# Kernel tuning notes

Measured on AMD Instinct MI355X. Metric: run time of the kernel, lower is better.

The kernel has to match this reference:

```python
import jax, jax.numpy as jnp
import numpy as np

OUT = 7  # STN crop size hard-coded as (7, 7) in the original build()


def gather_pairs(num_points):
    # replicates the pred_gather_indexes construction in build()
    pairs = [[0, 0]]
    si = 1
    while si + 2 < num_points:
        pairs.append([si, si])
        pairs.append([si + 1, si + 2])
        si += 3
    pairs.append([si, si])
    pairs.append([si + 1, si + 1])
    return np.asarray(pairs, dtype=np.int32)


def _sample_one(feat, theta):
    # feat [H,W,C], theta [6] = affine row-major 2x3; classic STN bilinear crop
    H, W, _ = feat.shape
    lin = jnp.linspace(-1.0, 1.0, OUT)
    gy, gx = jnp.meshgrid(lin, lin, indexing='ij')
    xs = theta[0] * gx + theta[1] * gy + theta[2]
    ys = theta[3] * gx + theta[4] * gy + theta[5]
    px = (xs + 1.0) * (W - 1) * 0.5
    py = (ys + 1.0) * (H - 1) * 0.5
    x0 = jnp.floor(px)
    y0 = jnp.floor(py)
    wx = px - x0
    wy = py - y0
    x0i = jnp.clip(x0, 0, W - 1).astype(jnp.int32)
    x1i = jnp.clip(x0 + 1, 0, W - 1).astype(jnp.int32)
    y0i = jnp.clip(y0, 0, H - 1).astype(jnp.int32)
    y1i = jnp.clip(y0 + 1, 0, H - 1).astype(jnp.int32)
    Ia = feat[y0i, x0i]
    Ib = feat[y1i, x0i]
    Ic = feat[y0i, x1i]
    Id = feat[y1i, x1i]
    wa = ((1 - wx) * (1 - wy))[..., None]
    wb = ((1 - wx) * wy)[..., None]
    wc = (wx * (1 - wy))[..., None]
    wd = (wx * wy)[..., None]
    return wa * Ia + wb * Ib + wc * Ic + wd * Id  # [OUT,OUT,C]

# vmap over boxes then over batch -> feat [B,H,W,C], theta [B,n,6] -> [B,n,7,7,C]
_sample = jax.vmap(jax.vmap(_sample_one, in_axes=(None, 0)), in_axes=(0, 0))


def _hierarchy(pred_prev, feat, W1, b1, W2, b2, W3, b3):
    B = pred_prev.shape[0]
    centers = (pred_prev[:, :-1] + pred_prev[:, 1:]) * 0.5
    diffs = (pred_prev[:, 1:] - pred_prev[:, :-1]) * 0.5
    cx, cy = centers[..., 0], centers[..., 1]
    dx, dy = diffs[..., 0], diffs[..., 1]
    # fixed (non-trainable) dense with constant kernel -> theta = [dx,-dy,-cx,dy,dx,-cy]
    theta = jnp.stack([dx, -dy, -cx, dy, dx, -cy], axis=-1)  # [B,n,6]
    theta = jax.lax.stop_gradient(theta)  # stop_gradient=True default
    rois = _sample(feat, theta)  # [B,n,7,7,C]
    n = theta.shape[1]
    x = rois.reshape(B * n, -1)
    f1 = jnp.tanh(x @ W1 + b1)
    f2 = jnp.tanh(f1 @ W2 + b2)
    f3 = f2 @ W3 + b3 + jnp.asarray([-1.0, 0.0, 0.0, 0.0, 1.0, 0.0], dtype=f2.dtype)
    npnt = n * 3
    pts = f3.reshape(B, npnt, 2)
    # fixed homography dense: (x,y) -> (x,y,-1)
    hom = jnp.concatenate([pts, -jnp.ones((B, npnt, 1), dtype=pts.dtype)], axis=-1)
    theta_e = jnp.repeat(theta, 3, axis=1).reshape(B, npnt, 2, 3)
    pt = jnp.einsum('bpij,bpj->bpi', theta_e, hom)  # [B,npnt,2]
    idx = gather_pairs(npnt)  # [m,2]
    pg = pt[:, idx]  # [B,m,2,2]
    return pg.mean(axis=2)  # [B,m,2]


def setup_inputs() -> dict:
    key = jax.random.key(0)
    ks = jax.random.split(key, 16)
    B = 32
    d = {
        'last_feature': jax.random.normal(ks[0], (B, 4096), jnp.float32),
        'conv4_3': jax.random.normal(ks[1], (B, 28, 28, 512), jnp.float32),
        'conv3_3': jax.random.normal(ks[2], (B, 56, 56, 256), jnp.float32),
        'conv2_2': jax.random.normal(ks[3], (B, 112, 112, 128), jnp.float32),
        'W_trans': jax.random.normal(ks[4], (4096, 18), jnp.float32) * 0.005,
        'b_trans': jnp.zeros((18,), jnp.float32),
    }
    C = [512, 256, 128]
    for h in range(3):
        kk = jax.random.split(ks[5 + h], 3)
        fan = OUT * OUT * C[h]
        d[f'W1_{h}'] = jax.random.normal(kk[0], (fan, 1024), jnp.float32) * 0.001
        d[f'b1_{h}'] = jnp.zeros((1024,), jnp.float32)
        d[f'W2_{h}'] = jax.random.normal(kk[1], (1024, 256), jnp.float32) * 0.02
        d[f'b2_{h}'] = jnp.zeros((256,), jnp.float32)
        d[f'W3_{h}'] = jax.random.normal(kk[2], (256, 6), jnp.float32) * 0.01
        d[f'b3_{h}'] = jnp.zeros((6,), jnp.float32)
    return d


def reference(last_feature, conv4_3, conv3_3, conv2_2, W_trans, b_trans,
              W1_0, b1_0, W2_0, b2_0, W3_0, b3_0,
              W1_1, b1_1, W2_1, b2_1, W3_1, b3_1,
              W1_2, b1_2, W2_2, b2_2, W3_2, b3_2):
    B = last_feature.shape[0]
    pred = (last_feature @ W_trans + b_trans).reshape(B, 9, 2)
    feats = [conv4_3, conv3_3, conv2_2]
    heads = [(W1_0, b1_0, W2_0, b2_0, W3_0, b3_0),
             (W1_1, b1_1, W2_1, b2_1, W3_1, b3_1),
             (W1_2, b1_2, W2_2, b2_2, W3_2, b3_2)]
    for h in range(3):
        pred = _hierarchy(pred, feats[h], *heads[h])
    return pred[:, :-1, :] * 6.0  # [B,64,2]
```

## Files before the change

kernel.cpp:

```cpp
#include <hip/hip_runtime.h>
#include <hip/hip_bf16.h>
#include <math.h>

typedef __attribute__((ext_vector_type(8))) short   short8;
typedef __attribute__((ext_vector_type(4))) float   floatx4;

#define OFF_PRED     0ULL
#define OFF_PTA      16384ULL
#define OFF_PTB      65536ULL
#define OFF_W2T      131072ULL
#define OFF_F1       2097152ULL
#define OFF_P2       4194304ULL
#define OFF_X        16777216ULL
#define OFF_P1       33554432ULL
#define OFF_W1T      67108864ULL

__device__ inline void pair_idx(int p, int Pn, int npnt, int& i1, int& i2) {
    if (p == 0) { i1 = i2 = 0; }
    else if (p >= Pn - 2) { i1 = i2 = npnt - (Pn - p); }
    else {
        int q = (p - 1) >> 1, r = (p - 1) & 1;
        int si = 1 + 3 * q;
        if (r == 0) { i1 = i2 = si; } else { i1 = si + 1; i2 = si + 2; }
    }
}
__device__ inline float2 pred_point(const float* pred0, const float* pt,
                                    int nsegP, int b, int p) {
    if (nsegP == 0) {
        const float* q = pred0 + ((size_t)b * 9 + p) * 2;
        return float2{q[0], q[1]};
    }
    int npnt = nsegP * 3, Pn = 2 * nsegP + 1;
    int i1, i2; pair_idx(p, Pn, npnt, i1, i2);
    const float* a = pt + ((size_t)b * npnt + i1) * 2;
    const float* c = pt + ((size_t)b * npnt + i2) * 2;
    return float2{0.5f * (a[0] + c[0]), 0.5f * (a[1] + c[1])};
}

struct SetupArgs {
    const float* W1s[3]; __hip_bfloat16* W1T[3]; int K[3];
    const float* W2s[3]; __hip_bfloat16* W2T[3];
    const float* lf; const float* Wt; const float* bt; float* pred;
};

__device__ inline void transpose_tile(const float* __restrict__ src,
                                      __hip_bfloat16* __restrict__ dst,
                                      int R, int C, int rowT, int colT,
                                      float (*tile)[33]) {
    int tx = threadIdx.x & 31, ty = threadIdx.x >> 5;
    int r0 = rowT * 32, c0 = colT * 32;
    #pragma unroll
    for (int k = 0; k < 4; ++k)
        tile[ty + k * 8][tx] = src[(size_t)(r0 + ty + k * 8) * C + c0 + tx];
    __syncthreads();
    #pragma unroll
    for (int k = 0; k < 4; ++k)
        dst[(size_t)(c0 + ty + k * 8) * R + r0 + tx] =
            __float2bfloat16(tile[tx][ty + k * 8]);
}

__global__ __launch_bounds__(256) void setup_kernel(SetupArgs a) {
    __shared__ float tile[32][33];
    int id = blockIdx.x;
    if (id < 43904) {
        int h = (id < 25088) ? 0 : (id < 37632 ? 1 : 2);
        int base = (h == 0) ? 0 : (h == 1 ? 25088 : 37632);
        int l = id - base;
        transpose_tile(a.W1s[h], a.W1T[h], a.K[h], 1024, l >> 5, l & 31, tile);
    } else if (id < 44672) {
        int l = id - 43904;
        int h = l >> 8; int t = l & 255;
        transpose_tile(a.W2s[h], a.W2T[h], 1024, 256, t >> 3, t & 7, tile);
    } else {
        int l = id - 44672;
        int wave = threadIdx.x >> 6, lane = threadIdx.x & 63;
        int task = l * 4 + wave;
        int j = task % 18, b = task / 18;
        const float* lfb = a.lf + (size_t)b * 4096;
        float acc = 0.f;
        for (int k = lane; k < 4096; k += 64)
            acc += lfb[k] * a.Wt[(size_t)k * 18 + j];
        #pragma unroll
        for (int off = 32; off >= 1; off >>= 1)
            acc += __shfl_xor(acc, off, 64);
        if (lane == 0) a.pred[b * 18 + j] = acc + a.bt[j];
    }
}

__global__ __launch_bounds__(256) void sample_kernel(
    const float* __restrict__ feat, int Wd, int lc,
    const float* __restrict__ pred0, const float* __restrict__ ptPrev, int nsegP,
    int lns, __hip_bfloat16* __restrict__ x)
{
    int nseg = 1 << lns;
    int blk = blockIdx.x;
    int i = blk & (nseg - 1), b = blk >> lns;
    float2 p0 = pred_point(pred0, ptPrev, nsegP, b, i);
    float2 p1 = pred_point(pred0, ptPrev, nsegP, b, i + 1);
    float cx = 0.5f * (p0.x + p1.x), cy = 0.5f * (p0.y + p1.y);
    float dx = 0.5f * (p1.x - p0.x), dy = 0.5f * (p1.y - p0.y);

    __shared__ float4 wv[49];
    __shared__ int4   ov[49];
    int t = threadIdx.x;
    int C = 1 << lc;
    if (t < 49) {
        int oy = t / 7, ox = t - oy * 7;
        float gx = (float)(ox - 3) * (1.f / 3.f);
        float gy = (float)(oy - 3) * (1.f / 3.f);
        float xs = dx * gx - dy * gy - cx;
        float ys = dy * gx + dx * gy - cy;
        float fW = (float)(Wd - 1);
        float px = (xs + 1.f) * fW * 0.5f;
        float py = (ys + 1.f) * fW * 0.5f;
        float x0f = floorf(px), y0f = floorf(py);
        float wx = px - x0f, wy = py - y0f;
        int xi0 = (int)fminf(fmaxf(x0f,       0.f), fW);
        int xi1 = (int)fminf(fmaxf(x0f + 1.f, 0.f), fW);
        int yi0 = (int)fminf(fmaxf(y0f,       0.f), fW);
        int yi1 = (int)fminf(fmaxf(y0f + 1.f, 0.f), fW);
        int c4 = C >> 2;
        ov[t] = int4{(yi0 * Wd + xi0) * c4, (yi1 * Wd + xi0) * c4,
                     (yi0 * Wd + xi1) * c4, (yi1 * Wd + xi1) * c4};
        wv[t] = float4{(1.f - wx) * (1.f - wy), (1.f - wx) * wy,
                       wx * (1.f - wy),         wx * wy};
    }
    __syncthreads();

    const float4* fb4 = (const float4*)(feat + (size_t)b * Wd * Wd * C);
    int c4 = 1 << (lc - 2);
    int total4 = 49 << (lc - 2);
    size_t rowbase = (size_t)blk * (49 << lc);
    for (int j = t; j < total4; j += 256) {
        int pix = j >> (lc - 2);
        int cc  = j & (c4 - 1);
        int4 o = ov[pix]; float4 w = wv[pix];
        float4 Ia = fb4[o.x + cc], Ib = fb4[o.y + cc];
        float4 Ic = fb4[o.z + cc], Id = fb4[o.w + cc];
        float4 v;
        v.x = w.x * Ia.x + w.y * Ib.x + w.z * Ic.x + w.w * Id.x;
        v.y = w.x * Ia.y + w.y * Ib.y + w.z * Ic.y + w.w * Id.y;
        v.z = w.x * Ia.z + w.y * Ib.z + w.z * Ic.z + w.w * Id.z;
        v.w = w.x * Ia.w + w.y * Ib.w + w.z * Ic.w + w.w * Id.w;
        __hip_bfloat16 h0 = __float2bfloat16(v.x), h1 = __float2bfloat16(v.y);
        __hip_bfloat16 h2 = __float2bfloat16(v.z), h3 = __float2bfloat16(v.w);
        ushort4 u = {*(unsigned short*)&h0, *(unsigned short*)&h1,
                     *(unsigned short*)&h2, *(unsigned short*)&h3};
        *(ushort4*)(x + rowbase + ((size_t)pix << lc) + cc * 4) = u;
    }
}

__global__ __launch_bounds__(256) void gemm_mfma4(
    const __hip_bfloat16* __restrict__ A, const __hip_bfloat16* __restrict__ Bt,
    float* __restrict__ P, int M, int N, int K, int slice)
{
    int lane = threadIdx.x & 63;
    int wave = threadIdx.x >> 6;
    int lo = lane & 15, hi = lane >> 4;
    int mt = blockIdx.x, nt = blockIdx.y * 4 + wave, s = blockIdx.z;
    const short* Ap = (const short*)A + (size_t)(mt * 64 + lo) * K + (size_t)s * slice + hi * 8;
    const short* Bp = (const short*)Bt + (size_t)(nt * 64 + lo) * K + (size_t)s * slice + hi * 8;

    floatx4 acc[4][4];
    #pragma unroll
    for (int a = 0; a < 4; ++a)
        #pragma unroll
        for (int b = 0; b < 4; ++b)
            acc[a][b] = floatx4{0.f, 0.f, 0.f, 0.f};

    short8 ca[4], cb[4], na[4], nb[4];
    int nch = slice >> 5;

#define LDF(da, db, koff)                                                     \
    {                                                                         \
        _Pragma("unroll")                                                     \
        for (int q = 0; q < 4; ++q)                                           \
            da[q] = *(const short8*)(Ap + (size_t)q * 16 * K + (koff));       \
        _Pragma("unroll")                                                     \
        for (int q = 0; q < 4; ++q)                                           \
            db[q] = *(const short8*)(Bp + (size_t)q * 16 * K + (koff));       \
    }
#define MM(da, db)                                                            \
    {                                                                         \
        _Pragma("unroll")                                                     \
        for (int mi = 0; mi < 4; ++mi)                                        \
            _Pragma("unroll")                                                 \
            for (int ni = 0; ni < 4; ++ni)                                    \
                acc[mi][ni] = __builtin_amdgcn_mfma_f32_16x16x32_bf16(        \
                    da[mi], db[ni], acc[mi][ni], 0, 0, 0);                    \
    }

    LDF(ca, cb, 0)
    for (int c = 0; c + 1 < nch; c += 2) {
        LDF(na, nb, (c + 1) * 32)
        MM(ca, cb)
        if (c + 2 < nch) LDF(ca, cb, (c + 2) * 32)
        MM(na, nb)
    }
    if (nch & 1) MM(ca, cb)

    #pragma unroll
    for (int mi = 0; mi < 4; ++mi) {
        int row0 = mt * 64 + mi * 16 + hi * 4;
        #pragma unroll
        for (int ni = 0; ni < 4; ++ni) {
            int col = nt * 64 + ni * 16 + lo;
            #pragma unroll
            for (int r = 0; r < 4; ++r)
                P[((size_t)s * M + row0 + r) * N + col] = acc[mi][ni][r];
        }
    }
#undef LDF
#undef MM
}

__global__ __launch_bounds__(256) void reduce_tanh_kernel(
    const float* __restrict__ P1, const float* __restrict__ b1,
    __hip_bfloat16* __restrict__ f1, int M, int S)
{
    int e = blockIdx.x * 256 + threadIdx.x;
    int n = e & 1023;
    float v = b1[n];
    size_t stride = (size_t)M * 1024;
    for (int s = 0; s < S; ++s) v += P1[(size_t)s * stride + e];
    f1[e] = __float2bfloat16(tanhf(v));
}

__global__ __launch_bounds__(64) void gemm3pts_kernel(
    const float* __restrict__ P2, const float* __restrict__ b2,
    const float* __restrict__ W3, const float* __restrict__ b3,
    const float* __restrict__ pred0, const float* __restrict__ ptPrev, int nsegP,
    float* __restrict__ pt, int lns, int M)
{
    int m = blockIdx.x;
    int lane = threadIdx.x;
    int nseg = 1 << lns;
    float acc[6] = {0.f, 0.f, 0.f, 0.f, 0.f, 0.f};
    #pragma unroll
    for (int q = 0; q < 4; ++q) {
        int k = lane + q * 64;
        float v = b2[k];
        #pragma unroll
        for (int s = 0; s < 8; ++s)
            v += P2[((size_t)s * M + m) * 256 + k];
        v = tanhf(v);
        const float* w = W3 + (size_t)k * 6;
        #pragma unroll
        for (int j = 0; j < 6; ++j) acc[j] += v * w[j];
    }
    #pragma unroll
    for (int j = 0; j < 6; ++j)
        #pragma unroll
        for (int off = 32; off >= 1; off >>= 1)
            acc[j] += __shfl_xor(acc[j], off, 64);
    if (lane == 0) {
        int i = m & (nseg - 1);
        int b = m >> lns;
        float2 p0 = pred_point(pred0, ptPrev, nsegP, b, i);
        float2 p1 = pred_point(pred0, ptPrev, nsegP, b, i + 1);
        float cx = 0.5f * (p0.x + p1.x), cy = 0.5f * (p0.y + p1.y);
        float dx = 0.5f * (p1.x - p0.x), dy = 0.5f * (p1.y - p0.y);
        float f[6];
        #pragma unroll
        for (int j = 0; j < 6; ++j) f[j] = acc[j] + b3[j];
        f[0] -= 1.f;
        f[4] += 1.f;
        int npnt = nseg * 3;
        size_t base = ((size_t)b * npnt + 3 * i) * 2;
        #pragma unroll
        for (int s = 0; s < 3; ++s) {
            float px = f[2 * s], py = f[2 * s + 1];
            pt[base + 2 * s]     = dx * px - dy * py + cx;
            pt[base + 2 * s + 1] = dy * px + dx * py + cy;
        }
    }
}

__global__ __launch_bounds__(256) void pairs_final_kernel(
    const float* __restrict__ pt, float* __restrict__ outp, int nsegP)
{
    int npnt = nsegP * 3;
    int Pn = 2 * nsegP + 1;
    int idx = blockIdx.x * 256 + threadIdx.x;
    int total = 32 * Pn * 2;
    if (idx >= total) return;
    int c = idx & 1;
    int t = idx >> 1;
    int p = t % Pn, b = t / Pn;
    int i1, i2; pair_idx(p, Pn, npnt, i1, i2);
    float v = 0.5f * (pt[((size_t)b * npnt + i1) * 2 + c] +
                      pt[((size_t)b * npnt + i2) * 2 + c]);
    if (p < Pn - 1) outp[((size_t)b * (Pn - 1) + p) * 2 + c] = 6.f * v;
}

extern "C" void kernel_launch(void* const* d_in, const int* in_sizes, int n_in,
                              void* d_out, int out_size, void* d_ws, size_t ws_size,
                              hipStream_t stream) {
    (void)in_sizes; (void)n_in; (void)out_size; (void)ws_size;
    const float* feats[3] = {(const float*)d_in[1], (const float*)d_in[2], (const float*)d_in[3]};

    char* ws = (char*)d_ws;
    float* predA = (float*)(ws + OFF_PRED);
    float* ptA   = (float*)(ws + OFF_PTA);
    float* ptB   = (float*)(ws + OFF_PTB);
    __hip_bfloat16* f1 = (__hip_bfloat16*)(ws + OFF_F1);
    float* P2          = (float*)(ws + OFF_P2);
    __hip_bfloat16* xb = (__hip_bfloat16*)(ws + OFF_X);
    float* P1          = (float*)(ws + OFF_P1);

    const int Ks[3]  = {25088, 12544, 6272};
    const int S1s[3] = {28, 14, 7};
    const int lcs[3] = {9, 8, 7};
    const int Hs[3]  = {28, 56, 112};
    const int lnss[3] = {3, 4, 5};

    SetupArgs sa;
    size_t w1off = 0;
    for (int h = 0; h < 3; ++h) {
        sa.W1s[h] = (const float*)d_in[6 + 6 * h];
        sa.W1T[h] = (__hip_bfloat16*)(ws + OFF_W1T + w1off);
        sa.K[h]   = Ks[h];
        w1off += (size_t)Ks[h] * 1024 * 2;
        sa.W2s[h] = (const float*)d_in[8 + 6 * h];
        sa.W2T[h] = (__hip_bfloat16*)(ws + OFF_W2T + (size_t)h * 524288);
    }
    sa.lf = (const float*)d_in[0];
    sa.Wt = (const float*)d_in[4];
    sa.bt = (const float*)d_in[5];
    sa.pred = predA;

    setup_kernel<<<dim3(44816), 256, 0, stream>>>(sa);

    float* pts[2] = {ptA, ptB};
    const float* ptPrev = nullptr;
    int nsegP = 0;
    for (int h = 0; h < 3; ++h) {
        int lns = lnss[h], nseg = 1 << lns, M = 32 * nseg;
        int K = Ks[h], S1 = S1s[h];
        const float* b1 = (const float*)d_in[7 + 6 * h];
        const float* b2 = (const float*)d_in[9 + 6 * h];
        const float* W3 = (const float*)d_in[10 + 6 * h];
        const float* b3 = (const float*)d_in[11 + 6 * h];

        sample_kernel<<<dim3(32 * nseg), 256, 0, stream>>>(
            feats[h], Hs[h], lcs[h], predA, ptPrev, nsegP, lns, xb);

        gemm_mfma4<<<dim3(M / 64, 4, S1), 256, 0, stream>>>(
            xb, sa.W1T[h], P1, M, 1024, K, K / S1);

        reduce_tanh_kernel<<<dim3(M * 1024 / 256), 256, 0, stream>>>(P1, b1, f1, M, S1);

        gemm_mfma4<<<dim3(M / 64, 1, 8), 256, 0, stream>>>(
            f1, sa.W2T[h], P2, M, 256, 1024, 128);

        float* ptCur = pts[h & 1];
        gemm3pts_kernel<<<dim3(M), 64, 0, stream>>>(
            P2, b2, W3, b3, predA, ptPrev, nsegP, ptCur, lns, M);

        ptPrev = ptCur; nsegP = nseg;
    }

    pairs_final_kernel<<<dim3((32 * 65 * 2 + 255) / 256), 256, 0, stream>>>(
        ptA, (float*)d_out, 32);
}
```

Before: 777.6 us.

## Triple-buffer GEMM loads, split sampling grid, vectorize reduce, pack gemm3 waves

The main GEMM moves from double to triple register buffering and raises wave priority around each MFMA burst, aiming to hide more global-load latency. The sample kernel splits each box's pixel-channel loop across a second grid dimension to get more blocks in flight. The split-K reduction now reads and writes four elements per thread with float4/ushort4 accesses, and gemm3pts packs four rows per 256-thread block. The extra buffers raise register pressure, which may lower occupancy, and the sample split recomputes the per-pixel offsets and weights in every block.

```diff
diff --git a/kernel.cpp b/kernel.cpp
--- a/kernel.cpp
+++ b/kernel.cpp
@@ -130,8 +130,10 @@
     const float4* fb4 = (const float4*)(feat + (size_t)b * Wd * Wd * C);
     int c4 = 1 << (lc - 2);
     int total4 = 49 << (lc - 2);
+    int chunk = total4 / gridDim.y;
+    int j0 = blockIdx.y * chunk;
     size_t rowbase = (size_t)blk * (49 << lc);
-    for (int j = t; j < total4; j += 256) {
+    for (int j = j0 + t; j < j0 + chunk; j += 256) {
         int pix = j >> (lc - 2);
         int cc  = j & (c4 - 1);
         int4 o = ov[pix]; float4 w = wv[pix];
@@ -168,7 +170,7 @@
         for (int b = 0; b < 4; ++b)
             acc[a][b] = floatx4{0.f, 0.f, 0.f, 0.f};
 
-    short8 ca[4], cb[4], na[4], nb[4];
+    short8 a0[4], b0[4], a1[4], b1[4], a2[4], b2[4];
     int nch = slice >> 5;
 
 #define LDF(da, db, koff)                                                     \
@@ -182,22 +184,46 @@
     }
 #define MM(da, db)                                                            \
     {                                                                         \
+        __builtin_amdgcn_s_setprio(1);                                        \
         _Pragma("unroll")                                                     \
         for (int mi = 0; mi < 4; ++mi)                                        \
             _Pragma("unroll")                                                 \
             for (int ni = 0; ni < 4; ++ni)                                    \
                 acc[mi][ni] = __builtin_amdgcn_mfma_f32_16x16x32_bf16(        \
                     da[mi], db[ni], acc[mi][ni], 0, 0, 0);                    \
-    }
-
-    LDF(ca, cb, 0)
-    for (int c = 0; c + 1 < nch; c += 2) {
-        LDF(na, nb, (c + 1) * 32)
-        MM(ca, cb)
-        if (c + 2 < nch) LDF(ca, cb, (c + 2) * 32)
-        MM(na, nb)
-    }
-    if (nch & 1) MM(ca, cb)
+        __builtin_amdgcn_s_setprio(0);                                        \
+    }
+
+    LDF(a0, b0, 0)
+    if (nch >= 2) LDF(a1, b1, 32)
+    int c = 0;
+    for (; c + 5 < nch; c += 3) {
+        LDF(a2, b2, (c + 2) * 32)
+        MM(a0, b0)
+        LDF(a0, b0, (c + 3) * 32)
+        MM(a1, b1)
+        LDF(a1, b1, (c + 4) * 32)
+        MM(a2, b2)
+    }
+    int r = nch - c;
+    if (r == 1) { MM(a0, b0) }
+    else if (r == 2) { MM(a0, b0) MM(a1, b1) }
+    else if (r == 3) {
+        LDF(a2, b2, (c + 2) * 32)
+        MM(a0, b0) MM(a1, b1) MM(a2, b2)
+    } else if (r == 4) {
+        LDF(a2, b2, (c + 2) * 32)
+        MM(a0, b0)
+        LDF(a0, b0, (c + 3) * 32)
+        MM(a1, b1) MM(a2, b2) MM(a0, b0)
+    } else {
+        LDF(a2, b2, (c + 2) * 32)
+        MM(a0, b0)
+        LDF(a0, b0, (c + 3) * 32)
+        MM(a1, b1)
+        LDF(a1, b1, (c + 4) * 32)
+        MM(a2, b2) MM(a0, b0) MM(a1, b1)
+    }
 
     #pragma unroll
     for (int mi = 0; mi < 4; ++mi) {
@@ -206,8 +232,8 @@
         for (int ni = 0; ni < 4; ++ni) {
             int col = nt * 64 + ni * 16 + lo;
             #pragma unroll
-            for (int r = 0; r < 4; ++r)
-                P[((size_t)s * M + row0 + r) * N + col] = acc[mi][ni][r];
+            for (int r2 = 0; r2 < 4; ++r2)
+                P[((size_t)s * M + row0 + r2) * N + col] = acc[mi][ni][r2];
         }
     }
 #undef LDF
@@ -218,22 +244,32 @@
     const float* __restrict__ P1, const float* __restrict__ b1,
     __hip_bfloat16* __restrict__ f1, int M, int S)
 {
-    int e = blockIdx.x * 256 + threadIdx.x;
-    int n = e & 1023;
-    float v = b1[n];
+    size_t e = ((size_t)blockIdx.x * 256 + threadIdx.x) * 4;
+    int n = (int)(e & 1023);
+    float4 v = *(const float4*)(b1 + n);
     size_t stride = (size_t)M * 1024;
-    for (int s = 0; s < S; ++s) v += P1[(size_t)s * stride + e];
-    f1[e] = __float2bfloat16(tanhf(v));
-}
-
-__global__ __launch_bounds__(64) void gemm3pts_kernel(
+    for (int s = 0; s < S; ++s) {
+        float4 p = *(const float4*)(P1 + (size_t)s * stride + e);
+        v.x += p.x; v.y += p.y; v.z += p.z; v.w += p.w;
+    }
+    __hip_bfloat16 h0 = __float2bfloat16(tanhf(v.x));
+    __hip_bfloat16 h1 = __float2bfloat16(tanhf(v.y));
+    __hip_bfloat16 h2 = __float2bfloat16(tanhf(v.z));
+    __hip_bfloat16 h3 = __float2bfloat16(tanhf(v.w));
+    ushort4 u = {*(unsigned short*)&h0, *(unsigned short*)&h1,
+                 *(unsigned short*)&h2, *(unsigned short*)&h3};
+    *(ushort4*)(f1 + e) = u;
+}
+
+__global__ __launch_bounds__(256) void gemm3pts_kernel(
     const float* __restrict__ P2, const float* __restrict__ b2,
     const float* __restrict__ W3, const float* __restrict__ b3,
     const float* __restrict__ pred0, const float* __restrict__ ptPrev, int nsegP,
     float* __restrict__ pt, int lns, int M)
 {
-    int m = blockIdx.x;
-    int lane = threadIdx.x;
+    int wave = threadIdx.x >> 6;
+    int m = blockIdx.x * 4 + wave;
+    int lane = threadIdx.x & 63;
     int nseg = 1 << lns;
     float acc[6] = {0.f, 0.f, 0.f, 0.f, 0.f, 0.f};
     #pragma unroll
@@ -313,6 +349,7 @@
     const int lcs[3] = {9, 8, 7};
     const int Hs[3]  = {28, 56, 112};
     const int lnss[3] = {3, 4, 5};
+    const int nspl[3] = {4, 4, 2};
 
     SetupArgs sa;
     size_t w1off = 0;
@@ -342,19 +379,19 @@
         const float* W3 = (const float*)d_in[10 + 6 * h];
         const float* b3 = (const float*)d_in[11 + 6 * h];
 
-        sample_kernel<<<dim3(32 * nseg), 256, 0, stream>>>(
+        sample_kernel<<<dim3(32 * nseg, nspl[h]), 256, 0, stream>>>(
             feats[h], Hs[h], lcs[h], predA, ptPrev, nsegP, lns, xb);
 
         gemm_mfma4<<<dim3(M / 64, 4, S1), 256, 0, stream>>>(
             xb, sa.W1T[h], P1, M, 1024, K, K / S1);
 
-        reduce_tanh_kernel<<<dim3(M * 1024 / 256), 256, 0, stream>>>(P1, b1, f1, M, S1);
+        reduce_tanh_kernel<<<dim3(M), 256, 0, stream>>>(P1, b1, f1, M, S1);
 
         gemm_mfma4<<<dim3(M / 64, 1, 8), 256, 0, stream>>>(
             f1, sa.W2T[h], P2, M, 256, 1024, 128);
 
         float* ptCur = pts[h & 1];
-        gemm3pts_kernel<<<dim3(M), 64, 0, stream>>>(
+        gemm3pts_kernel<<<dim3(M / 4), 256, 0, stream>>>(
             P2, b2, W3, b3, predA, ptPrev, nsegP, ptCur, lns, M);
 
         ptPrev = ptCur; nsegP = nseg;
```

Measured after the change: 758.8 us. 1.02x faster.
